# Kernel tuning notes

Hardware: AMD Instinct MI355X
Metric: run time of the kernel (lower is better)

## Reference

```python
import jax, jax.numpy as jnp
import numpy as np

B, S, D, H = 2, 2048, 1024, 16
HD = D // H  # head_dim = 64


def _rope_cos_sin(seq_len, head_dim, base=10000.0):
    # theta_i = base^(-2*(i-1)/dim), i = 1..dim/2
    i = jnp.arange(head_dim // 2, dtype=jnp.float32)
    theta = base ** (-2.0 * i / head_dim)
    m = jnp.arange(seq_len, dtype=jnp.float32)
    ang = jnp.outer(m, theta)  # [S, HD/2]
    return jnp.cos(ang), jnp.sin(ang)


def _apply_rope(x, cos, sin):
    # x: [B, S, H, HD]; pairs are consecutive elements (view_as_complex on (..., HD/2, 2))
    xr = x[..., 0::2]
    xi = x[..., 1::2]
    c = cos[None, :, None, :]
    s = sin[None, :, None, :]
    out_r = xr * c - xi * s
    out_i = xr * s + xi * c
    return jnp.stack([out_r, out_i], axis=-1).reshape(x.shape)


def setup_inputs() -> dict:
    key = jax.random.key(0)
    ks = jax.random.split(key, 7)
    sc = 1.0 / np.sqrt(D)
    return {
        "x": jax.random.normal(ks[0], (B, S, D), dtype=jnp.float32),
        "wq_w": jax.random.normal(ks[1], (D, D), dtype=jnp.float32) * sc,
        "wq_b": jax.random.normal(ks[2], (D,), dtype=jnp.float32) * 0.01,
        "wk_w": jax.random.normal(ks[3], (D, D), dtype=jnp.float32) * sc,
        "wk_b": jax.random.normal(ks[4], (D,), dtype=jnp.float32) * 0.01,
        "wv_w": jax.random.normal(ks[5], (D, D), dtype=jnp.float32) * sc,
        "wv_b": jax.random.normal(ks[6], (D,), dtype=jnp.float32) * 0.01,
    }


def reference(x, wq_w, wq_b, wk_w, wk_b, wv_w, wv_b):
    bs, seq_len, dim = x.shape
    # torch Linear: y = x @ W^T + b
    xq = (x @ wq_w.T + wq_b).reshape(bs, seq_len, H, HD)
    xk = (x @ wk_w.T + wk_b).reshape(bs, seq_len, H, HD)
    xv = (x @ wv_w.T + wv_b).reshape(bs, seq_len, H, HD)
    # RoPE (inference=True, start_pos=0): freqs for first seq_len positions
    cos, sin = _rope_cos_sin(seq_len, HD)
    xq = _apply_rope(xq, cos, sin)
    xk = _apply_rope(xk, cos, sin)
    # naive attention with full [B,H,S,S] score matrix, as in the original
    q = xq.transpose(0, 2, 1, 3)  # [B,H,S,HD]
    k = xk.transpose(0, 2, 1, 3)
    v = xv.transpose(0, 2, 1, 3)
    scores = jnp.einsum("bhqd,bhkd->bhqk", q, k) / np.sqrt(HD)
    attn = jax.nn.softmax(scores.astype(jnp.float32), axis=-1)
    out = jnp.einsum("bhqk,bhkd->bhqd", attn, v)
    return out.transpose(0, 2, 1, 3).reshape(bs, seq_len, dim)
```

## Files before the change

kernel.cpp:

```cpp
#include <hip/hip_runtime.h>


typedef __bf16 bf16;
typedef bf16  bf16x8 __attribute__((ext_vector_type(8)));
typedef bf16  bf16x4 __attribute__((ext_vector_type(4)));
typedef float f32x4  __attribute__((ext_vector_type(4)));
typedef float f32x16 __attribute__((ext_vector_type(16)));

typedef const __attribute__((address_space(1))) void* gptr_t;
typedef __attribute__((address_space(3))) void*       sptr_t;

__device__ __forceinline__ void gload_lds16(const void* g, void* l) {
  __builtin_amdgcn_global_load_lds((gptr_t)g, (sptr_t)l, 16, 0, 0);
}

__global__ __launch_bounds__(256) void prep_kernel(
    const float* __restrict__ x, const float* __restrict__ wq,
    const float* __restrict__ wk, const float* __restrict__ wv,
    bf16* __restrict__ xb, bf16* __restrict__ wqb, bf16* __restrict__ wkb,
    bf16* __restrict__ wvb, float* __restrict__ ctab, float* __restrict__ stab) {
  int g = blockIdx.x * 256 + threadIdx.x;
  const float* src;
  bf16* dst;
  int i;
  if (g < 1048576) { src = x; dst = xb; i = g; }
  else if (g < 1310720) { src = wq; dst = wqb; i = g - 1048576; }
  else if (g < 1572864) { src = wk; dst = wkb; i = g - 1310720; }
  else if (g < 1835008) { src = wv; dst = wvb; i = g - 1572864; }
  else {
    int idx = g - 1835008;
    if (idx < 65536) {
      int s = idx >> 5, p = idx & 31;
      double theta = exp2(-(double)p * (13.287712379549449 / 32.0));
      double ang = (double)s * theta;
      ctab[idx] = (float)cos(ang);
      stab[idx] = (float)sin(ang);
    }
    return;
  }
  const float4 v = reinterpret_cast<const float4*>(src)[i];
  bf16x4 o;
  o[0] = (bf16)v.x; o[1] = (bf16)v.y; o[2] = (bf16)v.z; o[3] = (bf16)v.w;
  reinterpret_cast<bf16x4*>(dst)[i] = o;
}

__global__ __launch_bounds__(256) void qkv_gemm_kernel(
    const bf16* __restrict__ xb, const bf16* __restrict__ wqb,
    const bf16* __restrict__ wkb, const bf16* __restrict__ wvb,
    const float* __restrict__ bq, const float* __restrict__ bk2,
    const float* __restrict__ bv, const float* __restrict__ ctab,
    const float* __restrict__ stab, bf16* __restrict__ qb,
    bf16* __restrict__ kb, bf16* __restrict__ vb) {
  const int z = blockIdx.z;
  const bf16* W = (z == 0) ? wqb : (z == 1) ? wkb : wvb;
  const float* bias = (z == 0) ? bq : (z == 1) ? bk2 : bv;
  bf16* dst = (z == 0) ? qb : (z == 1) ? kb : vb;

  __shared__ bf16 As[128 * 32];
  __shared__ bf16 Bs[128 * 32];

  const int tid = threadIdx.x;
  const int wid = tid >> 6;
  const int l = tid & 63;
  const int lg = l >> 4, lc = l & 15;
  const int wr = wid >> 1, wc = wid & 1;
  const int m0 = blockIdx.x * 128, n0 = blockIdx.y * 128;

  f32x4 acc[4][4] = {};

  const int arow = tid >> 2;
  const int acol = (tid & 3) * 8;
  const bf16* asrc = xb + (size_t)(m0 + arow) * 1024 + acol;
  const bf16* bsrc = W + (size_t)(n0 + arow) * 1024 + acol;
  char* alds = (char*)As + wid * 1024;
  char* blds = (char*)Bs + wid * 1024;

  for (int k0 = 0; k0 < 1024; k0 += 32) {
    gload_lds16(asrc + k0, alds);
    gload_lds16(asrc + 64 * 1024 + k0, alds + 4096);
    gload_lds16(bsrc + k0, blds);
    gload_lds16(bsrc + 64 * 1024 + k0, blds + 4096);
    __syncthreads();
    bf16x8 af[4], bfr[4];
#pragma unroll
    for (int i = 0; i < 4; ++i)
      af[i] = *reinterpret_cast<const bf16x8*>(
          (const char*)As + ((wr * 64 + i * 16 + lc) * 64 + lg * 16));
#pragma unroll
    for (int j = 0; j < 4; ++j)
      bfr[j] = *reinterpret_cast<const bf16x8*>(
          (const char*)Bs + ((wc * 64 + j * 16 + lc) * 64 + lg * 16));
#pragma unroll
    for (int i = 0; i < 4; ++i)
#pragma unroll
      for (int j = 0; j < 4; ++j)
        acc[i][j] = __builtin_amdgcn_mfma_f32_16x16x32_bf16(af[i], bfr[j],
                                                            acc[i][j], 0, 0, 0);
    __syncthreads();
  }

#pragma unroll
  for (int i = 0; i < 4; ++i)
#pragma unroll
    for (int j = 0; j < 4; ++j) {
      const int nb = n0 + wc * 64 + j * 16 + lc;
      const float bval = bias[nb];
#pragma unroll
      for (int r = 0; r < 4; ++r) {
        const int m = m0 + wr * 64 + i * 16 + lg * 4 + r;
        const float val = acc[i][j][r] + bval;
        if (z == 2) {
          dst[(size_t)m * 1024 + nb] = (bf16)val;
        } else {
          const int s = m & 2047;
          const int pi = (nb & 63) >> 1;
          const float c = ctab[s * 32 + pi];
          const float sn = stab[s * 32 + pi];
          const float part = __shfl_xor(val, 1, 64);
          float res = (nb & 1) ? fmaf(part, sn, val * c)
                               : fmaf(-part, sn, val * c);
          if (z == 0) res *= 0.18033688011112042f;
          dst[(size_t)m * 1024 + nb] = (bf16)res;
        }
      }
    }
}

__global__ __launch_bounds__(256) void vtrans_kernel(const bf16* __restrict__ vb,
                                                     bf16* __restrict__ vt) {
  __shared__ bf16 tile[64][65];
  const int bh = blockIdx.y, b = bh >> 4, h = bh & 15;
  const int s0 = blockIdx.x * 64;
  const int t = threadIdx.x;
#pragma unroll
  for (int idx = t; idx < 4096; idx += 256) {
    int r = idx >> 6, c = idx & 63;
    tile[r][c] = vb[(size_t)(b * 2048 + s0 + r) * 1024 + h * 64 + c];
  }
  __syncthreads();
#pragma unroll
  for (int idx = t; idx < 4096; idx += 256) {
    int d = idx >> 6, r = idx & 63;
    vt[(size_t)(bh * 64 + d) * 2048 + s0 + r] = tile[r][d];
  }
}

__device__ __forceinline__ unsigned pkbf(float a, float b) {
  union { bf16 h[2]; unsigned u; } t;
  t.h[0] = (bf16)a; t.h[1] = (bf16)b;
  return t.u;
}

__global__ __launch_bounds__(256) void attn_kernel(const bf16* __restrict__ qb,
                                                   const bf16* __restrict__ kb,
                                                   const bf16* __restrict__ vt,
                                                   float* __restrict__ out) {
  __shared__ float clds[2][64][34];

  const int tid = threadIdx.x;
  const int wid = tid >> 6;
  const int l = tid & 63;
  const int lc = l & 31;
  const int hi = l >> 5;
  const int bid = blockIdx.x;
  const int swz = (bid & 7) * 256 + (bid >> 3);
  const int bh = swz >> 6;
  const int qt = swz & 63;
  const int b = bh >> 4, h = bh & 15;
  const int q0 = qt * 32;

  const bf16* Q = qb + (size_t)(b * 2048 + q0) * 1024 + h * 64;
  const bf16* K = kb + (size_t)(b * 2048) * 1024 + h * 64;
  const bf16* V = vt + (size_t)bh * 64 * 2048;

  bf16x8 qf[4];
#pragma unroll
  for (int md = 0; md < 4; ++md)
    qf[md] = *reinterpret_cast<const bf16x8*>(Q + (size_t)lc * 1024 + md * 16 + hi * 8);

  f32x16 o0 = {};
  f32x16 o1 = {};
  float mrun = -1e30f, lrun = 0.f;
  const int sb = (hi ^ 1) * 2;

  const int kt_lo = wid * 16, kt_hi = kt_lo + 16;
  for (int kt = kt_lo; kt < kt_hi; ++kt) {
    const bf16* Krow = K + (size_t)(kt * 32 + lc) * 1024 + hi * 8;
    f32x16 s = {};
#pragma unroll
    for (int md = 0; md < 4; ++md) {
      bf16x8 kf = *reinterpret_cast<const bf16x8*>(Krow + md * 16);
      s = __builtin_amdgcn_mfma_f32_32x32x16_bf16(kf, qf[md], s, 0, 0, 0);
    }

    float tm = s[0];
#pragma unroll
    for (int r = 1; r < 16; ++r) tm = fmaxf(tm, s[r]);
    tm = fmaxf(tm, __shfl_xor(tm, 32, 64));
    if (!__all(tm <= mrun + 8.0f)) {
      const float mn = fmaxf(mrun, tm);
      const float corr = exp2f(mrun - mn);
      mrun = mn;
      lrun *= corr;
#pragma unroll
      for (int r = 0; r < 16; ++r) { o0[r] *= corr; o1[r] *= corr; }
    }
    float ts = 0.f;
#pragma unroll
    for (int r = 0; r < 16; ++r) {
      s[r] = exp2f(s[r] - mrun);
      ts += s[r];
    }
    ts += __shfl_xor(ts, 32, 64);
    lrun += ts;

    unsigned pw[8];
#pragma unroll
    for (int w = 0; w < 8; ++w) pw[w] = pkbf(s[2 * w], s[2 * w + 1]);

    unsigned rx0 = __shfl_xor(pw[sb + 0], 32, 64);
    unsigned rx1 = __shfl_xor(pw[sb + 1], 32, 64);
    unsigned rx2 = __shfl_xor(pw[4 + sb + 0], 32, 64);
    unsigned rx3 = __shfl_xor(pw[4 + sb + 1], 32, 64);

    union { unsigned u[4]; bf16x8 v; } bf0, bf1;
    if (hi == 0) {
      bf0.u[0] = pw[0]; bf0.u[1] = pw[1]; bf0.u[2] = rx0; bf0.u[3] = rx1;
      bf1.u[0] = pw[4]; bf1.u[1] = pw[5]; bf1.u[2] = rx2; bf1.u[3] = rx3;
    } else {
      bf0.u[0] = rx0; bf0.u[1] = rx1; bf0.u[2] = pw[2]; bf0.u[3] = pw[3];
      bf1.u[0] = rx2; bf1.u[1] = rx3; bf1.u[2] = pw[6]; bf1.u[3] = pw[7];
    }

    const bf16* Vb = V + (size_t)lc * 2048 + kt * 32 + hi * 8;
    bf16x8 vf00 = *reinterpret_cast<const bf16x8*>(Vb);
    bf16x8 vf01 = *reinterpret_cast<const bf16x8*>(Vb + 16);
    bf16x8 vf10 = *reinterpret_cast<const bf16x8*>(Vb + 32 * 2048);
    bf16x8 vf11 = *reinterpret_cast<const bf16x8*>(Vb + 32 * 2048 + 16);
    o0 = __builtin_amdgcn_mfma_f32_32x32x16_bf16(vf00, bf0.v, o0, 0, 0, 0);
    o0 = __builtin_amdgcn_mfma_f32_32x32x16_bf16(vf01, bf1.v, o0, 0, 0, 0);
    o1 = __builtin_amdgcn_mfma_f32_32x32x16_bf16(vf10, bf0.v, o1, 0, 0, 0);
    o1 = __builtin_amdgcn_mfma_f32_32x32x16_bf16(vf11, bf1.v, o1, 0, 0, 0);
  }

  if (wid >= 2) {
    float* dst = &clds[wid - 2][l][0];
#pragma unroll
    for (int r = 0; r < 16; ++r) { dst[r] = o0[r]; dst[16 + r] = o1[r]; }
    dst[32] = mrun; dst[33] = lrun;
  }
  __syncthreads();
  if (wid < 2) {
    const float* src = &clds[wid][l][0];
    const float mb = src[32], lb = src[33];
    const float M = fmaxf(mrun, mb);
    const float ca = exp2f(mrun - M), cb = exp2f(mb - M);
    mrun = M;
    lrun = lrun * ca + lb * cb;
#pragma unroll
    for (int r = 0; r < 16; ++r) {
      o0[r] = o0[r] * ca + src[r] * cb;
      o1[r] = o1[r] * ca + src[16 + r] * cb;
    }
  }
  __syncthreads();
  if (wid == 1) {
    float* dst = &clds[0][l][0];
#pragma unroll
    for (int r = 0; r < 16; ++r) { dst[r] = o0[r]; dst[16 + r] = o1[r]; }
    dst[32] = mrun; dst[33] = lrun;
  }
  __syncthreads();
  if (wid == 0) {
    const float* src = &clds[0][l][0];
    const float mb = src[32], lb = src[33];
    const float M = fmaxf(mrun, mb);
    const float ca = exp2f(mrun - M), cb = exp2f(mb - M);
    lrun = lrun * ca + lb * cb;
    const float inv = 1.f / lrun;
    float* orow = out + (size_t)(b * 2048 + q0 + lc) * 1024 + h * 64;
#pragma unroll
    for (int g = 0; g < 4; ++g) {
      f32x4 v0, v1;
#pragma unroll
      for (int e = 0; e < 4; ++e) {
        v0[e] = (o0[g * 4 + e] * ca + src[g * 4 + e] * cb) * inv;
        v1[e] = (o1[g * 4 + e] * ca + src[16 + g * 4 + e] * cb) * inv;
      }
      *reinterpret_cast<f32x4*>(orow + g * 8 + 4 * hi) = v0;
      *reinterpret_cast<f32x4*>(orow + 32 + g * 8 + 4 * hi) = v1;
    }
  }
}

extern "C" void kernel_launch(void* const* d_in, const int* in_sizes, int n_in,
                              void* d_out, int out_size, void* d_ws, size_t ws_size,
                              hipStream_t stream) {
  const float* x  = (const float*)d_in[0];
  const float* wq = (const float*)d_in[1];
  const float* bq = (const float*)d_in[2];
  const float* wk = (const float*)d_in[3];
  const float* bk = (const float*)d_in[4];
  const float* wv = (const float*)d_in[5];
  const float* bv = (const float*)d_in[6];
  float* out = (float*)d_out;

  char* ws = (char*)d_ws;
  bf16* xb  = (bf16*)(ws);
  bf16* wqb = (bf16*)(ws + 8388608);
  bf16* wkb = (bf16*)(ws + 10485760);
  bf16* wvb = (bf16*)(ws + 12582912);
  bf16* qb  = (bf16*)(ws + 14680064);
  bf16* kb  = (bf16*)(ws + 23068672);
  bf16* vb  = (bf16*)(ws + 31457280);
  bf16* vt  = (bf16*)(ws + 39845888);
  float* ctab = (float*)(ws + 48234496);
  float* stab = (float*)(ws + 48496640);

  prep_kernel<<<7424, 256, 0, stream>>>(x, wq, wk, wv, xb, wqb, wkb, wvb,
                                        ctab, stab);

  qkv_gemm_kernel<<<dim3(32, 8, 3), 256, 0, stream>>>(
      xb, wqb, wkb, wvb, bq, bk, bv, ctab, stab, qb, kb, vb);

  vtrans_kernel<<<dim3(32, 32), 256, 0, stream>>>(vb, vt);

  attn_kernel<<<2048, 256, 0, stream>>>(qb, kb, vt, out);
}
```

Before: 257.1 us.

## Share K/V tiles in LDS across four query-tile waves with double buffering

The attention kernel no longer splits the key range across four waves and merges partial softmax results. Each wave now owns its own 32-row query tile, so a block covers 128 queries and only 512 blocks are launched. K and V tiles of 64 keys are staged cooperatively into XOR-swizzled LDS with async global-to-LDS loads, double-buffered, and shared by all four waves. This is meant to cut redundant global K/V reads and remove the cross-wave LDS reduction. In exchange it adds a block barrier per key tile and gives fewer blocks (less parallelism) on the GPU.

```diff
diff --git a/kernel.cpp b/kernel.cpp
--- a/kernel.cpp
+++ b/kernel.cpp
@@ -155,7 +155,8 @@
                                                    const bf16* __restrict__ kb,
                                                    const bf16* __restrict__ vt,
                                                    float* __restrict__ out) {
-  __shared__ float clds[2][64][34];
+  __shared__ bf16 Kt[2][64][64];
+  __shared__ bf16 Vt[2][64][64];
 
   const int tid = threadIdx.x;
   const int wid = tid >> 6;
@@ -163,11 +164,11 @@
   const int lc = l & 31;
   const int hi = l >> 5;
   const int bid = blockIdx.x;
-  const int swz = (bid & 7) * 256 + (bid >> 3);
-  const int bh = swz >> 6;
-  const int qt = swz & 63;
+  const int swz = (bid & 7) * 64 + (bid >> 3);
+  const int bh = swz >> 4;
+  const int qt = swz & 15;
   const int b = bh >> 4, h = bh & 15;
-  const int q0 = qt * 32;
+  const int q0 = qt * 128 + wid * 32;
 
   const bf16* Q = qb + (size_t)(b * 2048 + q0) * 1024 + h * 64;
   const bf16* K = kb + (size_t)(b * 2048) * 1024 + h * 64;
@@ -177,119 +178,112 @@
 #pragma unroll
   for (int md = 0; md < 4; ++md)
     qf[md] = *reinterpret_cast<const bf16x8*>(Q + (size_t)lc * 1024 + md * 16 + hi * 8);
+
+  const int srow = l >> 3;
+  const int schk = (l & 7) ^ (srow & 7);
+  const bf16* ksrc0 = K + (size_t)(wid * 16 + srow) * 1024 + schk * 8;
+  const bf16* ksrc1 = ksrc0 + (size_t)8 * 1024;
+  const bf16* vsrc0 = V + (size_t)(wid * 16 + srow) * 2048 + schk * 8;
+  const bf16* vsrc1 = vsrc0 + (size_t)8 * 2048;
 
   f32x16 o0 = {};
   f32x16 o1 = {};
   float mrun = -1e30f, lrun = 0.f;
   const int sb = (hi ^ 1) * 2;
-
-  const int kt_lo = wid * 16, kt_hi = kt_lo + 16;
-  for (int kt = kt_lo; kt < kt_hi; ++kt) {
-    const bf16* Krow = K + (size_t)(kt * 32 + lc) * 1024 + hi * 8;
-    f32x16 s = {};
-#pragma unroll
-    for (int md = 0; md < 4; ++md) {
-      bf16x8 kf = *reinterpret_cast<const bf16x8*>(Krow + md * 16);
-      s = __builtin_amdgcn_mfma_f32_32x32x16_bf16(kf, qf[md], s, 0, 0, 0);
+  const int swzk = lc & 7;
+
+  gload_lds16(ksrc0, &Kt[0][wid * 16][0]);
+  gload_lds16(ksrc1, &Kt[0][wid * 16 + 8][0]);
+  gload_lds16(vsrc0, &Vt[0][wid * 16][0]);
+  gload_lds16(vsrc1, &Vt[0][wid * 16 + 8][0]);
+  __syncthreads();
+
+  int bb = 0;
+  for (int kt0 = 0; kt0 < 32; ++kt0) {
+    if (kt0 < 31) {
+      const size_t ko = (size_t)(kt0 + 1) * 64 * 1024;
+      const size_t vo = (size_t)(kt0 + 1) * 64;
+      gload_lds16(ksrc0 + ko, &Kt[bb ^ 1][wid * 16][0]);
+      gload_lds16(ksrc1 + ko, &Kt[bb ^ 1][wid * 16 + 8][0]);
+      gload_lds16(vsrc0 + vo, &Vt[bb ^ 1][wid * 16][0]);
+      gload_lds16(vsrc1 + vo, &Vt[bb ^ 1][wid * 16 + 8][0]);
     }
-
-    float tm = s[0];
-#pragma unroll
-    for (int r = 1; r < 16; ++r) tm = fmaxf(tm, s[r]);
-    tm = fmaxf(tm, __shfl_xor(tm, 32, 64));
-    if (!__all(tm <= mrun + 8.0f)) {
-      const float mn = fmaxf(mrun, tm);
-      const float corr = exp2f(mrun - mn);
-      mrun = mn;
-      lrun *= corr;
-#pragma unroll
-      for (int r = 0; r < 16; ++r) { o0[r] *= corr; o1[r] *= corr; }
+#pragma unroll
+    for (int sub = 0; sub < 2; ++sub) {
+      f32x16 s = {};
+#pragma unroll
+      for (int md = 0; md < 4; ++md) {
+        bf16x8 kf = *reinterpret_cast<const bf16x8*>(
+            &Kt[bb][sub * 32 + lc][(((md << 1) | hi) ^ swzk) << 3]);
+        s = __builtin_amdgcn_mfma_f32_32x32x16_bf16(kf, qf[md], s, 0, 0, 0);
+      }
+
+      float tm = s[0];
+#pragma unroll
+      for (int r = 1; r < 16; ++r) tm = fmaxf(tm, s[r]);
+      tm = fmaxf(tm, __shfl_xor(tm, 32, 64));
+      if (!__all(tm <= mrun + 8.0f)) {
+        const float mn = fmaxf(mrun, tm);
+        const float corr = exp2f(mrun - mn);
+        mrun = mn;
+        lrun *= corr;
+#pragma unroll
+        for (int r = 0; r < 16; ++r) { o0[r] *= corr; o1[r] *= corr; }
+      }
+      float ts = 0.f;
+#pragma unroll
+      for (int r = 0; r < 16; ++r) {
+        s[r] = exp2f(s[r] - mrun);
+        ts += s[r];
+      }
+      ts += __shfl_xor(ts, 32, 64);
+      lrun += ts;
+
+      unsigned pw[8];
+#pragma unroll
+      for (int w = 0; w < 8; ++w) pw[w] = pkbf(s[2 * w], s[2 * w + 1]);
+
+      unsigned rx0 = __shfl_xor(pw[sb + 0], 32, 64);
+      unsigned rx1 = __shfl_xor(pw[sb + 1], 32, 64);
+      unsigned rx2 = __shfl_xor(pw[4 + sb + 0], 32, 64);
+      unsigned rx3 = __shfl_xor(pw[4 + sb + 1], 32, 64);
+
+      union { unsigned u[4]; bf16x8 v; } bf0, bf1;
+      if (hi == 0) {
+        bf0.u[0] = pw[0]; bf0.u[1] = pw[1]; bf0.u[2] = rx0; bf0.u[3] = rx1;
+        bf1.u[0] = pw[4]; bf1.u[1] = pw[5]; bf1.u[2] = rx2; bf1.u[3] = rx3;
+      } else {
+        bf0.u[0] = rx0; bf0.u[1] = rx1; bf0.u[2] = pw[2]; bf0.u[3] = pw[3];
+        bf1.u[0] = rx2; bf1.u[1] = rx3; bf1.u[2] = pw[6]; bf1.u[3] = pw[7];
+      }
+
+      const int vc = sub * 4 + hi;
+      bf16x8 vf00 = *reinterpret_cast<const bf16x8*>(
+          &Vt[bb][lc][((vc ^ swzk)) << 3]);
+      bf16x8 vf01 = *reinterpret_cast<const bf16x8*>(
+          &Vt[bb][lc][(((vc + 2) ^ swzk)) << 3]);
+      bf16x8 vf10 = *reinterpret_cast<const bf16x8*>(
+          &Vt[bb][lc + 32][((vc ^ swzk)) << 3]);
+      bf16x8 vf11 = *reinterpret_cast<const bf16x8*>(
+          &Vt[bb][lc + 32][(((vc + 2) ^ swzk)) << 3]);
+      o0 = __builtin_amdgcn_mfma_f32_32x32x16_bf16(vf00, bf0.v, o0, 0, 0, 0);
+      o0 = __builtin_amdgcn_mfma_f32_32x32x16_bf16(vf01, bf1.v, o0, 0, 0, 0);
+      o1 = __builtin_amdgcn_mfma_f32_32x32x16_bf16(vf10, bf0.v, o1, 0, 0, 0);
+      o1 = __builtin_amdgcn_mfma_f32_32x32x16_bf16(vf11, bf1.v, o1, 0, 0, 0);
     }
-    float ts = 0.f;
-#pragma unroll
-    for (int r = 0; r < 16; ++r) {
-      s[r] = exp2f(s[r] - mrun);
-      ts += s[r];
-    }
-    ts += __shfl_xor(ts, 32, 64);
-    lrun += ts;
-
-    unsigned pw[8];
-#pragma unroll
-    for (int w = 0; w < 8; ++w) pw[w] = pkbf(s[2 * w], s[2 * w + 1]);
-
-    unsigned rx0 = __shfl_xor(pw[sb + 0], 32, 64);
-    unsigned rx1 = __shfl_xor(pw[sb + 1], 32, 64);
-    unsigned rx2 = __shfl_xor(pw[4 + sb + 0], 32, 64);
-    unsigned rx3 = __shfl_xor(pw[4 + sb + 1], 32, 64);
-
-    union { unsigned u[4]; bf16x8 v; } bf0, bf1;
-    if (hi == 0) {
-      bf0.u[0] = pw[0]; bf0.u[1] = pw[1]; bf0.u[2] = rx0; bf0.u[3] = rx1;
-      bf1.u[0] = pw[4]; bf1.u[1] = pw[5]; bf1.u[2] = rx2; bf1.u[3] = rx3;
-    } else {
-      bf0.u[0] = rx0; bf0.u[1] = rx1; bf0.u[2] = pw[2]; bf0.u[3] = pw[3];
-      bf1.u[0] = rx2; bf1.u[1] = rx3; bf1.u[2] = pw[6]; bf1.u[3] = pw[7];
-    }
-
-    const bf16* Vb = V + (size_t)lc * 2048 + kt * 32 + hi * 8;
-    bf16x8 vf00 = *reinterpret_cast<const bf16x8*>(Vb);
-    bf16x8 vf01 = *reinterpret_cast<const bf16x8*>(Vb + 16);
-    bf16x8 vf10 = *reinterpret_cast<const bf16x8*>(Vb + 32 * 2048);
-    bf16x8 vf11 = *reinterpret_cast<const bf16x8*>(Vb + 32 * 2048 + 16);
-    o0 = __builtin_amdgcn_mfma_f32_32x32x16_bf16(vf00, bf0.v, o0, 0, 0, 0);
-    o0 = __builtin_amdgcn_mfma_f32_32x32x16_bf16(vf01, bf1.v, o0, 0, 0, 0);
-    o1 = __builtin_amdgcn_mfma_f32_32x32x16_bf16(vf10, bf0.v, o1, 0, 0, 0);
-    o1 = __builtin_amdgcn_mfma_f32_32x32x16_bf16(vf11, bf1.v, o1, 0, 0, 0);
-  }
-
-  if (wid >= 2) {
-    float* dst = &clds[wid - 2][l][0];
-#pragma unroll
-    for (int r = 0; r < 16; ++r) { dst[r] = o0[r]; dst[16 + r] = o1[r]; }
-    dst[32] = mrun; dst[33] = lrun;
-  }
-  __syncthreads();
-  if (wid < 2) {
-    const float* src = &clds[wid][l][0];
-    const float mb = src[32], lb = src[33];
-    const float M = fmaxf(mrun, mb);
-    const float ca = exp2f(mrun - M), cb = exp2f(mb - M);
-    mrun = M;
-    lrun = lrun * ca + lb * cb;
-#pragma unroll
-    for (int r = 0; r < 16; ++r) {
-      o0[r] = o0[r] * ca + src[r] * cb;
-      o1[r] = o1[r] * ca + src[16 + r] * cb;
-    }
-  }
-  __syncthreads();
-  if (wid == 1) {
-    float* dst = &clds[0][l][0];
-#pragma unroll
-    for (int r = 0; r < 16; ++r) { dst[r] = o0[r]; dst[16 + r] = o1[r]; }
-    dst[32] = mrun; dst[33] = lrun;
-  }
-  __syncthreads();
-  if (wid == 0) {
-    const float* src = &clds[0][l][0];
-    const float mb = src[32], lb = src[33];
-    const float M = fmaxf(mrun, mb);
-    const float ca = exp2f(mrun - M), cb = exp2f(mb - M);
-    lrun = lrun * ca + lb * cb;
-    const float inv = 1.f / lrun;
-    float* orow = out + (size_t)(b * 2048 + q0 + lc) * 1024 + h * 64;
-#pragma unroll
-    for (int g = 0; g < 4; ++g) {
-      f32x4 v0, v1;
-#pragma unroll
-      for (int e = 0; e < 4; ++e) {
-        v0[e] = (o0[g * 4 + e] * ca + src[g * 4 + e] * cb) * inv;
-        v1[e] = (o1[g * 4 + e] * ca + src[16 + g * 4 + e] * cb) * inv;
-      }
-      *reinterpret_cast<f32x4*>(orow + g * 8 + 4 * hi) = v0;
-      *reinterpret_cast<f32x4*>(orow + 32 + g * 8 + 4 * hi) = v1;
-    }
+    __syncthreads();
+    bb ^= 1;
+  }
+
+  const float inv = 1.f / lrun;
+  float* orow = out + (size_t)(b * 2048 + q0 + lc) * 1024 + h * 64;
+#pragma unroll
+  for (int g = 0; g < 4; ++g) {
+    f32x4 v0, v1;
+#pragma unroll
+    for (int e = 0; e < 4; ++e) { v0[e] = o0[g * 4 + e] * inv; v1[e] = o1[g * 4 + e] * inv; }
+    *reinterpret_cast<f32x4*>(orow + g * 8 + 4 * hi) = v0;
+    *reinterpret_cast<f32x4*>(orow + 32 + g * 8 + 4 * hi) = v1;
   }
 }
 
@@ -325,5 +319,5 @@
 
   vtrans_kernel<<<dim3(32, 32), 256, 0, stream>>>(vb, vt);
 
-  attn_kernel<<<2048, 256, 0, stream>>>(qb, kb, vt, out);
-}
+  attn_kernel<<<512, 256, 0, stream>>>(qb, kb, vt, out);
+}
```

After: 218.9 us. 14.8% less time.
